# Kernel tuning notes

Measured on AMD Instinct MI355X. Metric: run time of the kernel, lower is better.

## Reference

```python
import jax, jax.numpy as jnp
import numpy as np

B, E, P, L, D = 16, 2048, 16384, 5, 64  # batch, num_edges, num node-pairs, max_path_distance, edge_dim
EPS = 1e-9


def setup_inputs() -> dict:
    key = jax.random.key(0)
    k1, k2, k3 = jax.random.split(key, 3)
    edge_embedding = jax.random.normal(k1, (B, E, D), dtype=jnp.float32)
    # -1 marks padding (unused path slots), valid entries in [0, E)
    edge_paths = jax.random.randint(k2, (B, P, L), -1, E, dtype=jnp.int64)
    edge_vector = jax.random.normal(k3, (L, D), dtype=jnp.float32)
    return {"edge_embedding": edge_embedding, "edge_paths": edge_paths, "edge_vector": edge_vector}


def reference(edge_embedding, edge_paths, edge_vector):
    # edge_embedding: (B, E, D); edge_paths: (B, P, L) int with -1 padding; edge_vector: (L, D)
    edge_mask = edge_paths == -1                                     # (B, P, L)
    clamped = jnp.clip(edge_paths, 0, None)
    # batched gather: out[b, p, l, :] = edge_embedding[b, clamped[b, p, l], :]
    gathered = jax.vmap(lambda emb, idx: emb[idx])(edge_embedding, clamped)  # (B, P, L, D)
    gathered = jnp.where(edge_mask[..., None], jnp.zeros((), gathered.dtype), gathered)
    path_lengths = (~edge_mask).sum(axis=-1).astype(edge_embedding.dtype) + EPS  # (B, P)
    enc = jnp.einsum('beld,ld->be', gathered, edge_vector)           # (B, P)
    return enc / path_lengths
```

## Files before the change

### kernel.cpp

```cpp
#include <hip/hip_runtime.h>
#include <hip/hip_bf16.h>

#define B 16
#define E 2048
#define P 16384
#define L 5
#define D 64
#define EPS 1e-9f

__global__ __launch_bounds__(256) void edge_proj_kernel(
    const float* __restrict__ emb, const float* __restrict__ ev,
    float* __restrict__ proj) {
    __shared__ float sev[L * D];
    for (int i = threadIdx.x; i < L * D; i += 256) sev[i] = ev[i];
    __syncthreads();

    int gid  = blockIdx.x * 256 + threadIdx.x;
    int row  = gid >> 1;
    int half = gid & 1;

    const float4* src = (const float4*)(emb + (size_t)row * D + half * 32);
    const float4* w4  = (const float4*)sev;

    float acc[L] = {0.f, 0.f, 0.f, 0.f, 0.f};
#pragma unroll
    for (int c = 0; c < 8; ++c) {
        float4 v = src[c];
#pragma unroll
        for (int l = 0; l < L; ++l) {
            float4 w = w4[l * 16 + half * 8 + c];
            acc[l] += v.x * w.x + v.y * w.y + v.z * w.z + v.w * w.w;
        }
    }
#pragma unroll
    for (int l = 0; l < L; ++l) acc[l] += __shfl_xor(acc[l], 1);

    if (half == 0) {
        float* p = proj + (size_t)row * L;
#pragma unroll
        for (int l = 0; l < L; ++l) p[l] = acc[l];
    }
}

__global__ __launch_bounds__(256) void edge_gather_kernel(
    const int* __restrict__ paths, const float* __restrict__ proj,
    float* __restrict__ out) {
    __shared__ float sproj[E * L];
    int b = blockIdx.x & 15;
    int g = blockIdx.x >> 4;

    const float4* src = (const float4*)(proj + (size_t)b * E * L);
    float4* dst = (float4*)sproj;
#pragma unroll
    for (int i = 0; i < (E * L) / 4 / 256; ++i)
        dst[threadIdx.x + i * 256] = src[threadIdx.x + i * 256];
    __syncthreads();

    int pbase = g * (P / 16);
#pragma unroll
    for (int k = 0; k < 4; ++k) {
        int p = pbase + k * 256 + threadIdx.x;
        const int* pp = paths + ((size_t)b * P + p) * L;
        float sum = 0.f;
        int cnt = 0;
#pragma unroll
        for (int l = 0; l < L; ++l) {
            int e = pp[l];
            bool valid = (e >= 0);
            int ec = valid ? e : 0;
            float v = sproj[ec * L + l];
            sum += valid ? v : 0.f;
            cnt += valid ? 1 : 0;
        }
        out[(size_t)b * P + p] = sum / ((float)cnt + EPS);
    }
}

extern "C" void kernel_launch(void* const* d_in, const int* in_sizes, int n_in,
                              void* d_out, int out_size, void* d_ws, size_t ws_size,
                              hipStream_t stream) {
    const float* emb   = (const float*)d_in[0];
    const int*   paths = (const int*)d_in[1];
    const float* ev    = (const float*)d_in[2];
    float* out  = (float*)d_out;
    float* proj = (float*)d_ws;

    edge_proj_kernel<<<(2 * B * E) / 256, 256, 0, stream>>>(emb, ev, proj);
    edge_gather_kernel<<<16 * B, 256, 0, stream>>>(paths, proj, out);
}
```

Baseline: 69.65 us.

## Fuse edge projection and path gather into one kernel with XCD-aware batch mapping

```diff
diff --git a/kernel.cpp b/kernel.cpp
--- a/kernel.cpp
+++ b/kernel.cpp
@@ -1,5 +1,4 @@
 #include <hip/hip_runtime.h>
-#include <hip/hip_bf16.h>
 
 #define B 16
 #define E 2048
@@ -8,67 +7,67 @@
 #define D 64
 #define EPS 1e-9f
 
-__global__ __launch_bounds__(256) void edge_proj_kernel(
-    const float* __restrict__ emb, const float* __restrict__ ev,
-    float* __restrict__ proj) {
+__global__ __launch_bounds__(512) void edge_fused_kernel(
+    const float* __restrict__ emb, const int* __restrict__ paths,
+    const float* __restrict__ ev, float* __restrict__ out) {
     __shared__ float sev[L * D];
-    for (int i = threadIdx.x; i < L * D; i += 256) sev[i] = ev[i];
+    __shared__ float sproj[E * L];
+
+    const int t    = threadIdx.x;
+    const int xcd  = blockIdx.x & 7;
+    const int slot = blockIdx.x >> 3;
+    const int b    = xcd * 2 + (slot & 1);
+    const int g    = slot >> 1;
+
+    int pidx[2][L];
+    const int pbase = g * (P / 16);
+#pragma unroll
+    for (int k = 0; k < 2; ++k) {
+        const int* pp = paths + ((size_t)b * P + pbase + k * 512 + t) * L;
+#pragma unroll
+        for (int l = 0; l < L; ++l) pidx[k][l] = pp[l];
+    }
+
+    for (int i = t; i < L * D; i += 512) sev[i] = ev[i];
     __syncthreads();
 
-    int gid  = blockIdx.x * 256 + threadIdx.x;
-    int row  = gid >> 1;
-    int half = gid & 1;
-
-    const float4* src = (const float4*)(emb + (size_t)row * D + half * 32);
-    const float4* w4  = (const float4*)sev;
-
-    float acc[L] = {0.f, 0.f, 0.f, 0.f, 0.f};
+    const int half = t & 1;
+    const int rt   = t >> 1;
+    const float4* w4 = (const float4*)sev;
 #pragma unroll
-    for (int c = 0; c < 8; ++c) {
-        float4 v = src[c];
+    for (int j = 0; j < E / 256; ++j) {
+        const int e = rt + j * 256;
+        const float4* src =
+            (const float4*)(emb + ((size_t)b * E + e) * D + half * 32);
+        float acc[L] = {0.f, 0.f, 0.f, 0.f, 0.f};
 #pragma unroll
-        for (int l = 0; l < L; ++l) {
-            float4 w = w4[l * 16 + half * 8 + c];
-            acc[l] += v.x * w.x + v.y * w.y + v.z * w.z + v.w * w.w;
+        for (int c = 0; c < 8; ++c) {
+            float4 v = src[c];
+#pragma unroll
+            for (int l = 0; l < L; ++l) {
+                float4 w = w4[l * 16 + half * 8 + c];
+                acc[l] += v.x * w.x + v.y * w.y + v.z * w.z + v.w * w.w;
+            }
+        }
+#pragma unroll
+        for (int l = 0; l < L; ++l) acc[l] += __shfl_xor(acc[l], 1);
+        if (half == 0) {
+#pragma unroll
+            for (int l = 0; l < L; ++l) sproj[e * L + l] = acc[l];
         }
     }
-#pragma unroll
-    for (int l = 0; l < L; ++l) acc[l] += __shfl_xor(acc[l], 1);
-
-    if (half == 0) {
-        float* p = proj + (size_t)row * L;
-#pragma unroll
-        for (int l = 0; l < L; ++l) p[l] = acc[l];
-    }
-}
-
-__global__ __launch_bounds__(256) void edge_gather_kernel(
-    const int* __restrict__ paths, const float* __restrict__ proj,
-    float* __restrict__ out) {
-    __shared__ float sproj[E * L];
-    int b = blockIdx.x & 15;
-    int g = blockIdx.x >> 4;
-
-    const float4* src = (const float4*)(proj + (size_t)b * E * L);
-    float4* dst = (float4*)sproj;
-#pragma unroll
-    for (int i = 0; i < (E * L) / 4 / 256; ++i)
-        dst[threadIdx.x + i * 256] = src[threadIdx.x + i * 256];
     __syncthreads();
 
-    int pbase = g * (P / 16);
 #pragma unroll
-    for (int k = 0; k < 4; ++k) {
-        int p = pbase + k * 256 + threadIdx.x;
-        const int* pp = paths + ((size_t)b * P + p) * L;
+    for (int k = 0; k < 2; ++k) {
+        const int p = pbase + k * 512 + t;
         float sum = 0.f;
         int cnt = 0;
 #pragma unroll
         for (int l = 0; l < L; ++l) {
-            int e = pp[l];
-            bool valid = (e >= 0);
-            int ec = valid ? e : 0;
-            float v = sproj[ec * L + l];
+            const int e = pidx[k][l];
+            const bool valid = (e >= 0);
+            const float v = sproj[(valid ? e : 0) * L + l];
             sum += valid ? v : 0.f;
             cnt += valid ? 1 : 0;
         }
@@ -82,9 +81,8 @@
     const float* emb   = (const float*)d_in[0];
     const int*   paths = (const int*)d_in[1];
     const float* ev    = (const float*)d_in[2];
-    float* out  = (float*)d_out;
-    float* proj = (float*)d_ws;
+    float* out = (float*)d_out;
+    (void)d_ws; (void)ws_size;
 
-    edge_proj_kernel<<<(2 * B * E) / 256, 256, 0, stream>>>(emb, ev, proj);
-    edge_gather_kernel<<<16 * B, 256, 0, stream>>>(paths, proj, out);
+    edge_fused_kernel<<<256, 512, 0, stream>>>(emb, paths, ev, out);
 }
```

Result: slower. 82.19 us (+18.0%).

## Vectorize path index loads, prefetch before LDS fill, split projection rows four ways

Applied to the files above, without the earlier changes.

```diff
diff --git a/kernel.cpp b/kernel.cpp
--- a/kernel.cpp
+++ b/kernel.cpp
@@ -1,5 +1,4 @@
 #include <hip/hip_runtime.h>
-#include <hip/hip_bf16.h>
 
 #define B 16
 #define E 2048
@@ -11,31 +10,34 @@
 __global__ __launch_bounds__(256) void edge_proj_kernel(
     const float* __restrict__ emb, const float* __restrict__ ev,
     float* __restrict__ proj) {
-    __shared__ float sev[L * D];
-    for (int i = threadIdx.x; i < L * D; i += 256) sev[i] = ev[i];
-    __syncthreads();
+    const int gid = blockIdx.x * 256 + threadIdx.x;
+    const int row = gid >> 2;
+    const int q   = gid & 3;
 
-    int gid  = blockIdx.x * 256 + threadIdx.x;
-    int row  = gid >> 1;
-    int half = gid & 1;
+    const float4* src = (const float4*)(emb + (size_t)row * D + q * 16);
+    const float4* w4  = (const float4*)ev;
 
-    const float4* src = (const float4*)(emb + (size_t)row * D + half * 32);
-    const float4* w4  = (const float4*)sev;
+    float4 v[4];
+#pragma unroll
+    for (int c = 0; c < 4; ++c) v[c] = src[c];
 
-    float acc[L] = {0.f, 0.f, 0.f, 0.f, 0.f};
+    float acc[L];
 #pragma unroll
-    for (int c = 0; c < 8; ++c) {
-        float4 v = src[c];
+    for (int l = 0; l < L; ++l) {
+        float s = 0.f;
 #pragma unroll
-        for (int l = 0; l < L; ++l) {
-            float4 w = w4[l * 16 + half * 8 + c];
-            acc[l] += v.x * w.x + v.y * w.y + v.z * w.z + v.w * w.w;
+        for (int c = 0; c < 4; ++c) {
+            const float4 w = w4[l * 16 + q * 4 + c];
+            s += v[c].x * w.x + v[c].y * w.y + v[c].z * w.z + v[c].w * w.w;
         }
+        acc[l] = s;
     }
 #pragma unroll
-    for (int l = 0; l < L; ++l) acc[l] += __shfl_xor(acc[l], 1);
-
-    if (half == 0) {
+    for (int l = 0; l < L; ++l) {
+        acc[l] += __shfl_xor(acc[l], 1);
+        acc[l] += __shfl_xor(acc[l], 2);
+    }
+    if (q == 0) {
         float* p = proj + (size_t)row * L;
 #pragma unroll
         for (int l = 0; l < L; ++l) p[l] = acc[l];
@@ -46,34 +48,49 @@
     const int* __restrict__ paths, const float* __restrict__ proj,
     float* __restrict__ out) {
     __shared__ float sproj[E * L];
-    int b = blockIdx.x & 15;
-    int g = blockIdx.x >> 4;
+    const int t = threadIdx.x;
+    const int b = blockIdx.x & 15;
+    const int g = blockIdx.x >> 4;
+
+    const int pbase = g * (P / 16);
+    const int4* pp = (const int4*)(paths + ((size_t)b * P + pbase) * L);
+    int4 pv[5];
+#pragma unroll
+    for (int i = 0; i < 5; ++i) pv[i] = pp[t * 5 + i];
 
     const float4* src = (const float4*)(proj + (size_t)b * E * L);
     float4* dst = (float4*)sproj;
 #pragma unroll
     for (int i = 0; i < (E * L) / 4 / 256; ++i)
-        dst[threadIdx.x + i * 256] = src[threadIdx.x + i * 256];
+        dst[t + i * 256] = src[t + i * 256];
     __syncthreads();
 
-    int pbase = g * (P / 16);
+    int pidx[20];
+#pragma unroll
+    for (int i = 0; i < 5; ++i) {
+        pidx[i * 4 + 0] = pv[i].x;
+        pidx[i * 4 + 1] = pv[i].y;
+        pidx[i * 4 + 2] = pv[i].z;
+        pidx[i * 4 + 3] = pv[i].w;
+    }
+
+    float4 res;
+    float* rp = (float*)&res;
 #pragma unroll
     for (int k = 0; k < 4; ++k) {
-        int p = pbase + k * 256 + threadIdx.x;
-        const int* pp = paths + ((size_t)b * P + p) * L;
         float sum = 0.f;
         int cnt = 0;
 #pragma unroll
         for (int l = 0; l < L; ++l) {
-            int e = pp[l];
-            bool valid = (e >= 0);
-            int ec = valid ? e : 0;
-            float v = sproj[ec * L + l];
+            const int e = pidx[k * 5 + l];
+            const bool valid = (e >= 0);
+            const float v = sproj[(valid ? e : 0) * L + l];
             sum += valid ? v : 0.f;
             cnt += valid ? 1 : 0;
         }
-        out[(size_t)b * P + p] = sum / ((float)cnt + EPS);
+        rp[k] = sum / ((float)cnt + EPS);
     }
+    *(float4*)(out + (size_t)b * P + pbase + t * 4) = res;
 }
 
 extern "C" void kernel_launch(void* const* d_in, const int* in_sizes, int n_in,
@@ -85,6 +102,6 @@
     float* out  = (float*)d_out;
     float* proj = (float*)d_ws;
 
-    edge_proj_kernel<<<(2 * B * E) / 256, 256, 0, stream>>>(emb, ev, proj);
+    edge_proj_kernel<<<(4 * B * E) / 256, 256, 0, stream>>>(emb, ev, proj);
     edge_gather_kernel<<<16 * B, 256, 0, stream>>>(paths, proj, out);
 }
```

After: 69.35 us. Within noise of the previous version (-0.4%).
